# Optimization experiments

Measured on AMD Instinct MI355X. Metric: run time of the kernel, lower is better.

The kernel has to match this reference:

```python
import jax, jax.numpy as jnp
import numpy as np

NUM_HEADS = 16
KV_CHANNELS = 128
MASK_FILL = -10000.0  # TE attention_mask_func fill value


def setup_inputs() -> dict:
    key = jax.random.key(0)
    k1, k2, k3 = jax.random.split(key, 3)
    S, B, H = 2048, 2, 2048
    hidden_states = jax.random.normal(k1, (S, B, H), dtype=jnp.float32)
    attention_mask = jnp.zeros((B, 1, S, S), dtype=bool)  # True = masked out
    qkv_weight = jax.random.normal(k2, (H, 3 * H), dtype=jnp.float32) * (1.0 / np.sqrt(H))
    qkv_bias = jnp.zeros((3 * H,), dtype=jnp.float32)
    proj_weight = jax.random.normal(k3, (H, H), dtype=jnp.float32) * (1.0 / np.sqrt(H))
    proj_bias = jnp.zeros((H,), dtype=jnp.float32)
    return {
        "hidden_states": hidden_states,
        "attention_mask": attention_mask,
        "qkv_weight": qkv_weight,
        "qkv_bias": qkv_bias,
        "proj_weight": proj_weight,
        "proj_bias": proj_bias,
    }


def reference(hidden_states, attention_mask, qkv_weight, qkv_bias, proj_weight, proj_bias):
    S, B, H = hidden_states.shape
    nh, d = NUM_HEADS, KV_CHANNELS
    # QKV GEMM: [s,b,H] @ [H,3H] -> [s,b,3H] -> [s,b,nh,3d] -> split
    mixed = hidden_states @ qkv_weight + qkv_bias
    mixed = mixed.reshape(S, B, nh, 3 * d)
    q, k, v = jnp.split(mixed, 3, axis=-1)  # each [s,b,nh,d]
    # BMM1 with 1/sqrt(d) scaling (layer_number=None -> no layer scaling)
    norm_factor = jnp.asarray(np.sqrt(d), dtype=hidden_states.dtype)
    scores = jnp.einsum("sbhd,tbhd->bhst", q, k) / norm_factor  # [b,nh,s,s]
    # causal mask (future positions masked) OR'd with provided bool padding mask
    causal = ~jnp.tril(jnp.ones((S, S), dtype=bool))  # True above diagonal
    mask = jnp.logical_or(causal[None, None], attention_mask)
    scores = jnp.where(mask, jnp.asarray(MASK_FILL, scores.dtype), scores)
    probs = jax.nn.softmax(scores, axis=-1)
    # dropout is identity in eval mode (training=False)
    # BMM2: [b,nh,s,t] x [t,b,nh,d] -> [s,b,nh,d] -> [s,b,H]
    context = jnp.einsum("bhst,tbhd->sbhd", probs, v).reshape(S, B, H)
    # output projection; TE Dense(use_bias=False, return_bias=True) returns bias
    out = context @ proj_weight
    return out, proj_bias
```

## Files before the change

kernel.cpp:

```cpp
#include <hip/hip_runtime.h>
#include <cstdint>
#include <math.h>

#define S_LEN 2048
#define BATCH 2
#define HID   2048
#define NHEAD 16
#define DHEAD 128

typedef _Float16 h8 __attribute__((ext_vector_type(8)));
typedef _Float16 h4 __attribute__((ext_vector_type(4)));
typedef float f32x4 __attribute__((ext_vector_type(4)));

__device__ __forceinline__ void gload16(const void* g, void* l) {
  __builtin_amdgcn_global_load_lds(
      (const __attribute__((address_space(1))) unsigned int*)g,
      (__attribute__((address_space(3))) unsigned int*)l, 16, 0, 0);
}

template <bool HAS_BIAS, bool OUT_HALF>
__global__ __launch_bounds__(256) void gemm_mfma(
    const _Float16* __restrict__ A, const _Float16* __restrict__ Bt,
    const float* __restrict__ bias, void* __restrict__ Cout, int M, int N,
    int K) {
  __shared__ _Float16 As[128 * 32];
  __shared__ _Float16 Bs[128 * 32];
  const int tid = threadIdx.x;
  const int wave = tid >> 6, lane = tid & 63;
  const int ln = lane & 15, quad = lane >> 4;
  const int wm = wave & 1, wn = wave >> 1;
  const int bm = blockIdx.y * 128, bn = blockIdx.x * 128;

  const int sr = lane >> 2;
  const int sk = (lane & 3) * 8;
  const _Float16* ga0 = A + (size_t)(bm + 32 * wave + sr) * K + sk;
  const _Float16* ga1 = A + (size_t)(bm + 32 * wave + 16 + sr) * K + sk;
  const _Float16* gb0 = Bt + (size_t)(bn + 32 * wave + sr) * K + sk;
  const _Float16* gb1 = Bt + (size_t)(bn + 32 * wave + 16 + sr) * K + sk;
  _Float16* la0 = As + 1024 * wave;
  _Float16* la1 = As + 1024 * wave + 512;
  _Float16* lb0 = Bs + 1024 * wave;
  _Float16* lb1 = Bs + 1024 * wave + 512;

  f32x4 acc[4][4];
#pragma unroll
  for (int i = 0; i < 4; i++)
#pragma unroll
    for (int j = 0; j < 4; j++) acc[i][j] = (f32x4){0.f, 0.f, 0.f, 0.f};

  for (int kt = 0; kt < K; kt += 32) {
    __syncthreads();
    gload16(ga0 + kt, la0);
    gload16(ga1 + kt, la1);
    gload16(gb0 + kt, lb0);
    gload16(gb1 + kt, lb1);
    __syncthreads();

    h8 af[4], bf[4];
#pragma unroll
    for (int mt = 0; mt < 4; mt++)
      af[mt] = *(const h8*)&As[(wm * 64 + mt * 16 + ln) * 32 + quad * 8];
#pragma unroll
    for (int nt = 0; nt < 4; nt++)
      bf[nt] = *(const h8*)&Bs[(wn * 64 + nt * 16 + ln) * 32 + quad * 8];
#pragma unroll
    for (int mt = 0; mt < 4; mt++)
#pragma unroll
      for (int nt = 0; nt < 4; nt++)
        acc[mt][nt] = __builtin_amdgcn_mfma_f32_16x16x32_f16(
            af[mt], bf[nt], acc[mt][nt], 0, 0, 0);
  }

#pragma unroll
  for (int mt = 0; mt < 4; mt++) {
#pragma unroll
    for (int r = 0; r < 4; r++) {
      const size_t row = (size_t)(bm + wm * 64 + mt * 16 + quad * 4 + r);
#pragma unroll
      for (int nt = 0; nt < 4; nt++) {
        const int col = bn + wn * 64 + nt * 16 + ln;
        float v = acc[mt][nt][r];
        if (HAS_BIAS) v += bias[col];
        if (OUT_HALF)
          ((_Float16*)Cout)[row * N + col] = (_Float16)v;
        else
          ((float*)Cout)[row * N + col] = v;
      }
    }
  }
}

__global__ __launch_bounds__(256) void transpose_cvt(
    const float* __restrict__ in, _Float16* __restrict__ out, int K, int N) {
  __shared__ float t[64][65];
  const int bn = blockIdx.x * 64, bk = blockIdx.y * 64;
  const int l = threadIdx.x & 63, g = threadIdx.x >> 6;
#pragma unroll
  for (int i = 0; i < 16; i++) {
    int r = g + 4 * i;
    t[r][l] = in[(size_t)(bk + r) * N + bn + l];
  }
  __syncthreads();
#pragma unroll
  for (int i = 0; i < 16; i++) {
    int r = g + 4 * i;
    out[(size_t)(bn + r) * K + bk + l] = (_Float16)t[l][r];
  }
}

__global__ __launch_bounds__(256) void cvt_fp16(const float* __restrict__ in,
                                                _Float16* __restrict__ out,
                                                int n4) {
  int i = blockIdx.x * blockDim.x + threadIdx.x;
  if (i < n4) {
    float4 v = ((const float4*)in)[i];
    h4 o = {(_Float16)v.x, (_Float16)v.y, (_Float16)v.z, (_Float16)v.w};
    *(h4*)&out[4 * (size_t)i] = o;
  }
}

__global__ __launch_bounds__(256) void pack_kv(
    const _Float16* __restrict__ mixed, _Float16* __restrict__ KP,
    _Float16* __restrict__ VP) {
  __shared__ _Float16 Tv[128 * 40];
  const int kt = blockIdx.x;
  const int z = blockIdx.y;
  const int kb = kt * 32;
  const int tid = threadIdx.x;
  const size_t RS = (size_t)BATCH * NHEAD * 384;
  const _Float16* base = mixed + (size_t)z * 384;

  {
    const int r = tid >> 3, d0 = (tid & 7) * 16;
    const _Float16* src = base + (size_t)(kb + r) * RS + 256 + d0;
    h8 v0 = *(const h8*)src;
    h8 v1 = *(const h8*)(src + 8);
#pragma unroll
    for (int e = 0; e < 8; e++) Tv[(d0 + e) * 40 + r] = v0[e];
#pragma unroll
    for (int e = 0; e < 8; e++) Tv[(d0 + 8 + e) * 40 + r] = v1[e];
  }
  __syncthreads();

  const size_t tb = ((size_t)z * 64 + kt) * 8 * 512;
#pragma unroll
  for (int c = 0; c < 2; c++) {
    const int idx = tid + 256 * c;
    const int i = idx >> 6, l = idx & 63;
    const int ln = l & 15, quad = l >> 4;
    {
      const int jn = i >> 2, kq = i & 3;
      h8 v = *(const h8*)(base + (size_t)(kb + 16 * jn + ln) * RS + 128 +
                          32 * kq + 8 * quad);
      *(h8*)&KP[tb + (size_t)i * 512 + l * 8] = v;
    }
    {
      h8 v = *(const h8*)&Tv[(16 * i + ln) * 40 + 8 * quad];
      *(h8*)&VP[tb + (size_t)i * 512 + l * 8] = v;
    }
  }
}

__global__ __launch_bounds__(256) void flash_attn_v7(
    const _Float16* __restrict__ mixed, const _Float16* __restrict__ KP,
    const _Float16* __restrict__ VP, const unsigned char* __restrict__ mask,
    _Float16* __restrict__ ctx) {
  const int qt = (int)gridDim.x - 1 - (int)blockIdx.x;
  const int h = blockIdx.y, b = blockIdx.z;
  const int z = b * NHEAD + h;
  const int qb = qt * 64;
  const int tid = threadIdx.x;
  const int wave = tid >> 6, lane = tid & 63;
  const int ln = lane & 15, quad = lane >> 4;

  __shared__ _Float16 Kbuf[2][8 * 512];
  __shared__ _Float16 Vbuf[2][8 * 512];
  __shared__ _Float16 St[4][16 * 40];

  const size_t RS = (size_t)BATCH * NHEAD * 384;
  const _Float16* base = mixed + (size_t)z * 384;
  const unsigned char* mbase = mask + (size_t)b * S_LEN * S_LEN;
  const float scale = 0.08838834764831845f;

  h8 qfrag[4];
  {
    const size_t row = (size_t)(qb + 16 * wave + ln);
#pragma unroll
    for (int kq = 0; kq < 4; kq++) {
      h8 v = *(const h8*)(base + row * RS + 32 * kq + 8 * quad);
#pragma unroll
      for (int j = 0; j < 8; j++) v[j] = (_Float16)((float)v[j] * scale);
      qfrag[kq] = v;
    }
  }

  f32x4 o[8];
#pragma unroll
  for (int nt = 0; nt < 8; nt++) o[nt] = (f32x4){0.f, 0.f, 0.f, 0.f};
  float lpart[4] = {0.f, 0.f, 0.f, 0.f};

  const int ntiles = 2 * qt + 2;

  const size_t zt = (size_t)z * 64;
#define STAGE(kt_, buf_)                                                   \
  {                                                                        \
    const size_t tbk = (zt + (kt_)) * (8 * 512) + lane * 8;                \
    _Pragma("unroll") for (int c = 0; c < 2; c++) {                        \
      const int ch = 2 * wave + c;                                         \
      gload16(KP + tbk + ch * 512, &Kbuf[buf_][ch * 512]);                 \
      gload16(VP + tbk + ch * 512, &Vbuf[buf_][ch * 512]);                 \
    }                                                                      \
  }

  STAGE(0, 0)

  for (int kt = 0; kt < ntiles; kt++) {
    const int kb = kt * 32;
    const int cur = kt & 1;
    __syncthreads();

    if (kt + 1 < ntiles) STAGE(kt + 1, cur ^ 1)

    unsigned char mreg[4][2];
#pragma unroll
    for (int r = 0; r < 4; r++)
#pragma unroll
      for (int jn = 0; jn < 2; jn++)
        mreg[r][jn] = mbase[(size_t)(qb + 16 * wave + 4 * quad + r) * S_LEN +
                            kb + 16 * jn + ln];

    f32x4 s[2];
    s[0] = (f32x4){0.f, 0.f, 0.f, 0.f};
    s[1] = (f32x4){0.f, 0.f, 0.f, 0.f};
#pragma unroll
    for (int kq = 0; kq < 4; kq++) {
#pragma unroll
      for (int jn = 0; jn < 2; jn++) {
        h8 bk = *(const h8*)&Kbuf[cur][(jn * 4 + kq) * 512 + lane * 8];
        s[jn] = __builtin_amdgcn_mfma_f32_16x16x32_f16(qfrag[kq], bk, s[jn], 0,
                                                       0, 0);
      }
    }

#pragma unroll
    for (int jn = 0; jn < 2; jn++)
#pragma unroll
      for (int r = 0; r < 4; r++) {
        const int grow = qb + 16 * wave + 4 * quad + r;
        const int gcol = kb + 16 * jn + ln;
        const float sv = ((gcol > grow) || mreg[r][jn]) ? -10000.0f : s[jn][r];
        const float p = __expf(sv);
        lpart[r] += p;
        St[wave][(4 * quad + r) * 40 + 16 * jn + ln] = (_Float16)p;
      }
    __threadfence_block();

    {
      h8 ap = *(const h8*)&St[wave][ln * 40 + 8 * quad];
#pragma unroll
      for (int nt = 0; nt < 8; nt++) {
        h8 bv = *(const h8*)&Vbuf[cur][nt * 512 + lane * 8];
        o[nt] = __builtin_amdgcn_mfma_f32_16x16x32_f16(ap, bv, o[nt], 0, 0, 0);
      }
    }
  }
#undef STAGE

#pragma unroll
  for (int r = 0; r < 4; r++) {
    float l = lpart[r];
#pragma unroll
    for (int off = 8; off >= 1; off >>= 1) l += __shfl_xor(l, off, 16);
    const float inv_l = 1.0f / l;
    const size_t row_g = (size_t)(qb + 16 * wave + 4 * quad + r);
    _Float16* dst = ctx + (row_g * BATCH + b) * HID + h * DHEAD;
#pragma unroll
    for (int nt = 0; nt < 8; nt++)
      dst[16 * nt + ln] = (_Float16)(o[nt][r] * inv_l);
  }
}

__global__ void copy_bias(const float* __restrict__ src,
                          float* __restrict__ dst) {
  int i = blockIdx.x * blockDim.x + threadIdx.x;
  if (i < HID) dst[i] = src[i];
}

extern "C" void kernel_launch(void* const* d_in, const int* in_sizes, int n_in,
                              void* d_out, int out_size, void* d_ws,
                              size_t ws_size, hipStream_t stream) {
  (void)in_sizes;
  (void)n_in;
  const float* hs = (const float*)d_in[0];
  const unsigned char* mask = (const unsigned char*)d_in[1];
  const float* qkv_w = (const float*)d_in[2];
  const float* qkv_b = (const float*)d_in[3];
  const float* proj_w = (const float*)d_in[4];
  const float* proj_b = (const float*)d_in[5];
  float* out = (float*)d_out;

  const size_t M = (size_t)S_LEN * BATCH;
  const size_t mixed_e = M * 3 * HID;
  const size_t qkvwt_e = (size_t)3 * HID * HID;
  const size_t hsh_e = M * HID;
  const size_t projwt_e = (size_t)HID * HID;
  const size_t ctx_e = M * HID;
  const size_t need =
      (mixed_e + qkvwt_e + hsh_e + projwt_e + ctx_e) * sizeof(_Float16);
  if (ws_size < need) return;

  _Float16* mixed = (_Float16*)d_ws;
  _Float16* qkv_wt = mixed + mixed_e;
  _Float16* hs_h = qkv_wt + qkvwt_e;
  _Float16* proj_wt = hs_h + hsh_e;
  _Float16* ctx = proj_wt + projwt_e;
  _Float16* KP = hs_h;
  _Float16* VP = qkv_wt;

  cvt_fp16<<<(int)(hsh_e / 4 / 256), 256, 0, stream>>>(hs, hs_h,
                                                       (int)(hsh_e / 4));
  transpose_cvt<<<dim3(3 * HID / 64, HID / 64), 256, 0, stream>>>(
      qkv_w, qkv_wt, HID, 3 * HID);
  transpose_cvt<<<dim3(HID / 64, HID / 64), 256, 0, stream>>>(
      proj_w, proj_wt, HID, HID);

  gemm_mfma<true, true><<<dim3(3 * HID / 128, M / 128), 256, 0, stream>>>(
      hs_h, qkv_wt, qkv_b, mixed, (int)M, 3 * HID, HID);

  pack_kv<<<dim3(S_LEN / 32, BATCH * NHEAD), 256, 0, stream>>>(mixed, KP, VP);

  flash_attn_v7<<<dim3(S_LEN / 64, NHEAD, BATCH), 256, 0, stream>>>(
      mixed, KP, VP, mask, ctx);

  gemm_mfma<false, false><<<dim3(HID / 128, M / 128), 256, 0, stream>>>(
      ctx, proj_wt, nullptr, out, (int)M, HID, HID);

  copy_bias<<<(HID + 255) / 256, 256, 0, stream>>>(proj_b, out + M * HID);
}
```

Before: 475.9 us.

## Replace GEMM with 256x256 tile, double-buffered, swizzled LDS, interleaved MFMA pipeline

Replaces the 128x128 single-buffer GEMM with a 512-thread 256x256-tile kernel. It uses K-step 64, double-buffered LDS, an XOR swizzle against bank conflicts, and a schedule that interleaves global-to-LDS prefetch with four MFMA quadrants under s_setprio. The aim is to hide global load latency and raise arithmetic intensity for both the QKV and output projection GEMMs. In exchange it uses much more LDS and registers per block, and launches fewer blocks (96 and 32), which may underfill the CUs for the smaller GEMM.

```diff
diff --git a/kernel.cpp b/kernel.cpp
--- a/kernel.cpp
+++ b/kernel.cpp
@@ -19,67 +19,143 @@
 }
 
 template <bool HAS_BIAS, bool OUT_HALF>
-__global__ __launch_bounds__(256) void gemm_mfma(
+__global__ __launch_bounds__(512) void gemm_256(
     const _Float16* __restrict__ A, const _Float16* __restrict__ Bt,
     const float* __restrict__ bias, void* __restrict__ Cout, int M, int N,
     int K) {
-  __shared__ _Float16 As[128 * 32];
-  __shared__ _Float16 Bs[128 * 32];
-  const int tid = threadIdx.x;
+  __shared__ _Float16 LA[2][2][8192];
+  __shared__ _Float16 LB[2][2][8192];
+  const int tid = (int)threadIdx.x;
   const int wave = tid >> 6, lane = tid & 63;
   const int ln = lane & 15, quad = lane >> 4;
-  const int wm = wave & 1, wn = wave >> 1;
-  const int bm = blockIdx.y * 128, bn = blockIdx.x * 128;
-
-  const int sr = lane >> 2;
-  const int sk = (lane & 3) * 8;
-  const _Float16* ga0 = A + (size_t)(bm + 32 * wave + sr) * K + sk;
-  const _Float16* ga1 = A + (size_t)(bm + 32 * wave + 16 + sr) * K + sk;
-  const _Float16* gb0 = Bt + (size_t)(bn + 32 * wave + sr) * K + sk;
-  const _Float16* gb1 = Bt + (size_t)(bn + 32 * wave + 16 + sr) * K + sk;
-  _Float16* la0 = As + 1024 * wave;
-  _Float16* la1 = As + 1024 * wave + 512;
-  _Float16* lb0 = Bs + 1024 * wave;
-  _Float16* lb1 = Bs + 1024 * wave + 512;
-
-  f32x4 acc[4][4];
-#pragma unroll
-  for (int i = 0; i < 4; i++)
-#pragma unroll
-    for (int j = 0; j < 4; j++) acc[i][j] = (f32x4){0.f, 0.f, 0.f, 0.f};
-
-  for (int kt = 0; kt < K; kt += 32) {
-    __syncthreads();
-    gload16(ga0 + kt, la0);
-    gload16(ga1 + kt, la1);
-    gload16(gb0 + kt, lb0);
-    gload16(gb1 + kt, lb1);
-    __syncthreads();
-
-    h8 af[4], bf[4];
-#pragma unroll
-    for (int mt = 0; mt < 4; mt++)
-      af[mt] = *(const h8*)&As[(wm * 64 + mt * 16 + ln) * 32 + quad * 8];
-#pragma unroll
-    for (int nt = 0; nt < 4; nt++)
-      bf[nt] = *(const h8*)&Bs[(wn * 64 + nt * 16 + ln) * 32 + quad * 8];
-#pragma unroll
-    for (int mt = 0; mt < 4; mt++)
-#pragma unroll
-      for (int nt = 0; nt < 4; nt++)
-        acc[mt][nt] = __builtin_amdgcn_mfma_f32_16x16x32_f16(
-            af[mt], bf[nt], acc[mt][nt], 0, 0, 0);
-  }
-
-#pragma unroll
-  for (int mt = 0; mt < 4; mt++) {
+  const int wm = wave >> 2, wn = wave & 3;
+  const int bm = (int)blockIdx.y * 256, bn = (int)blockIdx.x * 256;
+  const int NT = K >> 6;
+
+  const int rA = wave * 16 + (lane >> 3);
+  const int gc8 = ((lane & 7) ^ (lane >> 3)) * 8;
+  const uint32_t oA00 = (uint32_t)(bm + rA) * (uint32_t)K + (uint32_t)gc8;
+  const uint32_t oA01 = oA00 + (uint32_t)(8 * K);
+  const uint32_t oA10 = oA00 + (uint32_t)(128 * K);
+  const uint32_t oA11 = oA10 + (uint32_t)(8 * K);
+  const uint32_t oB00 = (uint32_t)(bn + rA) * (uint32_t)K + (uint32_t)gc8;
+  const uint32_t oB01 = oB00 + (uint32_t)(8 * K);
+  const uint32_t oB10 = oB00 + (uint32_t)(128 * K);
+  const uint32_t oB11 = oB10 + (uint32_t)(8 * K);
+  const int cw0 = wave * 1024;
+  const int cw1 = cw0 + 512;
+
+#define STAGE_A(h_, bb_, u_)                                           \
+  {                                                                    \
+    gload16(A + (oA##h_##0 + (uint32_t)(u_)*64u), &LA[bb_][h_][cw0]);  \
+    gload16(A + (oA##h_##1 + (uint32_t)(u_)*64u), &LA[bb_][h_][cw1]);  \
+  }
+#define STAGE_B(h_, bb_, u_)                                           \
+  {                                                                    \
+    gload16(Bt + (oB##h_##0 + (uint32_t)(u_)*64u), &LB[bb_][h_][cw0]); \
+    gload16(Bt + (oB##h_##1 + (uint32_t)(u_)*64u), &LB[bb_][h_][cw1]); \
+  }
+
+  const int arow = ln * 64;
+  const int sc0 = ((quad ^ (ln & 7))) * 8;
+  const int sc1 = (((4 + quad) ^ (ln & 7))) * 8;
+  const int bro = (wn & 1) * 4096;
+
+  f32x4 acc[8][4];
+#pragma unroll
+  for (int m = 0; m < 8; m++)
+#pragma unroll
+    for (int n = 0; n < 4; n++) acc[m][n] = (f32x4){0.f, 0.f, 0.f, 0.f};
+  h8 aLo[4][2], aHi[4][2], bF[4][2];
+
+#define QUAD(aF_, mo_, no_)                                                  \
+  _Pragma("unroll") for (int mm_ = 0; mm_ < 4; mm_++)                        \
+      _Pragma("unroll") for (int nn_ = 0; nn_ < 2; nn_++) {                  \
+    acc[(mo_) + mm_][(no_) + nn_] = __builtin_amdgcn_mfma_f32_16x16x32_f16(  \
+        aF_[mm_][0], bF[(no_) + nn_][0], acc[(mo_) + mm_][(no_) + nn_], 0,   \
+        0, 0);                                                               \
+    acc[(mo_) + mm_][(no_) + nn_] = __builtin_amdgcn_mfma_f32_16x16x32_f16(  \
+        aF_[mm_][1], bF[(no_) + nn_][1], acc[(mo_) + mm_][(no_) + nn_], 0,   \
+        0, 0);                                                               \
+  }
+
+  STAGE_A(0, 0, 0) STAGE_A(1, 0, 0) STAGE_B(0, 0, 0) STAGE_B(1, 0, 0)
+  STAGE_A(0, 1, 1) STAGE_B(0, 1, 1) STAGE_B(1, 1, 1)
+  asm volatile("s_waitcnt vmcnt(6)" ::: "memory");
+  __builtin_amdgcn_s_barrier();
+
+  for (int u = 0; u < NT; ++u) {
+    const int bb = u & 1;
+
+#pragma unroll
+    for (int m = 0; m < 4; m++) {
+      aLo[m][0] = *(const h8*)&LA[bb][wm][m * 1024 + arow + sc0];
+      aLo[m][1] = *(const h8*)&LA[bb][wm][m * 1024 + arow + sc1];
+    }
+    if (u + 1 < NT) STAGE_A(1, bb ^ 1, u + 1)
+    __builtin_amdgcn_s_barrier();
+    asm volatile("s_waitcnt lgkmcnt(0)" ::: "memory");
+    if (u) {
+      __builtin_amdgcn_s_setprio(1);
+      QUAD(aHi, 4, 2)
+      __builtin_amdgcn_s_setprio(0);
+    }
+    __builtin_amdgcn_s_barrier();
+
+#pragma unroll
+    for (int n = 0; n < 4; n++) {
+      bF[n][0] = *(const h8*)&LB[bb][wn >> 1][bro + n * 1024 + arow + sc0];
+      bF[n][1] = *(const h8*)&LB[bb][wn >> 1][bro + n * 1024 + arow + sc1];
+    }
+    __builtin_amdgcn_s_barrier();
+    asm volatile("s_waitcnt lgkmcnt(0)" ::: "memory");
+    __builtin_amdgcn_s_setprio(1);
+    QUAD(aLo, 0, 0)
+    __builtin_amdgcn_s_setprio(0);
+    __builtin_amdgcn_s_barrier();
+
+#pragma unroll
+    for (int m = 0; m < 4; m++) {
+      aHi[m][0] = *(const h8*)&LA[bb][wm][(m + 4) * 1024 + arow + sc0];
+      aHi[m][1] = *(const h8*)&LA[bb][wm][(m + 4) * 1024 + arow + sc1];
+    }
+    if (u + 2 < NT) { STAGE_B(0, bb, u + 2) STAGE_B(1, bb, u + 2) }
+    __builtin_amdgcn_s_barrier();
+    asm volatile("s_waitcnt lgkmcnt(0)" ::: "memory");
+    __builtin_amdgcn_s_setprio(1);
+    QUAD(aHi, 4, 0)
+    __builtin_amdgcn_s_setprio(0);
+    __builtin_amdgcn_s_barrier();
+
+    if (u + 2 < NT) {
+      STAGE_A(0, bb, u + 2)
+      asm volatile("s_waitcnt vmcnt(6)" ::: "memory");
+    } else if (u + 1 < NT) {
+      asm volatile("s_waitcnt vmcnt(0)" ::: "memory");
+    }
+    __builtin_amdgcn_s_barrier();
+    __builtin_amdgcn_s_setprio(1);
+    QUAD(aLo, 0, 2)
+    __builtin_amdgcn_s_setprio(0);
+    __builtin_amdgcn_s_barrier();
+  }
+
+  __builtin_amdgcn_s_setprio(1);
+  QUAD(aHi, 4, 2)
+  __builtin_amdgcn_s_setprio(0);
+#undef QUAD
+#undef STAGE_A
+#undef STAGE_B
+
+#pragma unroll
+  for (int m = 0; m < 8; m++) {
 #pragma unroll
     for (int r = 0; r < 4; r++) {
-      const size_t row = (size_t)(bm + wm * 64 + mt * 16 + quad * 4 + r);
-#pragma unroll
-      for (int nt = 0; nt < 4; nt++) {
-        const int col = bn + wn * 64 + nt * 16 + ln;
-        float v = acc[mt][nt][r];
+      const size_t row = (size_t)(bm + wm * 128 + m * 16 + quad * 4 + r);
+#pragma unroll
+      for (int n = 0; n < 4; n++) {
+        const int col = bn + wn * 64 + n * 16 + ln;
+        float v = acc[m][n][r];
         if (HAS_BIAS) v += bias[col];
         if (OUT_HALF)
           ((_Float16*)Cout)[row * N + col] = (_Float16)v;
@@ -324,7 +400,7 @@
   transpose_cvt<<<dim3(HID / 64, HID / 64), 256, 0, stream>>>(
       proj_w, proj_wt, HID, HID);
 
-  gemm_mfma<true, true><<<dim3(3 * HID / 128, M / 128), 256, 0, stream>>>(
+  gemm_256<true, true><<<dim3(3 * HID / 256, M / 256), 512, 0, stream>>>(
       hs_h, qkv_wt, qkv_b, mixed, (int)M, 3 * HID, HID);
 
   pack_kv<<<dim3(S_LEN / 32, BATCH * NHEAD), 256, 0, stream>>>(mixed, KP, VP);
@@ -332,7 +408,7 @@
   flash_attn_v7<<<dim3(S_LEN / 64, NHEAD, BATCH), 256, 0, stream>>>(
       mixed, KP, VP, mask, ctx);
 
-  gemm_mfma<false, false><<<dim3(HID / 128, M / 128), 256, 0, stream>>>(
+  gemm_256<false, false><<<dim3(HID / 256, M / 256), 512, 0, stream>>>(
       ctx, proj_wt, nullptr, out, (int)M, HID, HID);
 
   copy_bias<<<(HID + 255) / 256, 256, 0, stream>>>(proj_b, out + M * HID);
```

After: 457.9 us. -3.8%, faster.
